# Kernel tuning notes

Measured on AMD Instinct MI355X. Metric: run time of the kernel, lower is better.

The kernel has to match this reference:

```python
import jax, jax.numpy as jnp
import numpy as np

E = 1024
H = 16
D = E // H
T = 1024
S = 1024
B = 8
MASK_FILL = 1e-30  # note: module fills masked scores with 1e-30, NOT -inf


def setup_inputs() -> dict:
    key = jax.random.key(0)
    ks = jax.random.split(key, 8)
    inp = {
        "query1": jax.random.normal(ks[0], (T, B, E), jnp.float32),
        "query2": jax.random.normal(ks[1], (T, B, E), jnp.float32),
        "key": jax.random.normal(ks[2], (S, B, E), jnp.float32),
        "value": jax.random.normal(ks[3], (S, B, E), jnp.float32),
        # causal mask: True = masked
        "attn_mask": jnp.triu(jnp.ones((T, S), jnp.bool_), k=1),
        # xavier-uniform-ish weights (torch stores Linear weight as [out, in])
        "q_w": jax.random.uniform(ks[4], (E, E), jnp.float32, -1, 1) * np.sqrt(6.0 / (2 * E)),
        "k_w": jax.random.uniform(ks[5], (E, E), jnp.float32, -1, 1) * np.sqrt(6.0 / (2 * E)),
        "v_w": jax.random.uniform(ks[6], (E, E), jnp.float32, -1, 1) * np.sqrt(6.0 / (2 * E)),
        "out_w": jax.random.uniform(ks[7], (E, E), jnp.float32, -1, 1) * np.sqrt(6.0 / (2 * E)),
    }
    return inp


def _split_heads(x):
    # [L, B, E] -> [B, H, L, D]
    L = x.shape[0]
    return x.reshape(L, B, H, D).transpose(1, 2, 0, 3)


def reference(query1, query2, key, value, attn_mask, q_w, k_w, v_w, out_w):
    scaling = float(D) ** -0.5
    q1 = _split_heads(query1 @ q_w.T) * scaling  # [B,H,T,D]
    q2 = _split_heads(query2 @ q_w.T) * scaling
    k = _split_heads(key @ k_w.T)                # [B,H,S,D]
    v = _split_heads(value @ v_w.T)

    # ---- stream s (second query stream attends first) ----
    scores_s = jnp.einsum("bhtd,bhsd->bhts", q2, k)
    scores_s = jnp.where(attn_mask[None, None], MASK_FILL, scores_s)
    probs_s = jax.nn.softmax(scores_s, axis=-1)
    o_s = jnp.einsum("bhts,bhsd->bhtd", probs_s, v)  # [B,H,T,D]

    # k/v update between passes (requires T == S)
    k2 = k + o_s
    v2 = v + o_s

    # ---- stream d ----
    scores_d = jnp.einsum("bhtd,bhsd->bhts", q1, k2)
    scores_d = jnp.where(attn_mask[None, None], MASK_FILL, scores_d)
    probs_d = jax.nn.softmax(scores_d, axis=-1)
    o_d = jnp.einsum("bhts,bhsd->bhtd", probs_d, v2)

    def _merge_and_proj(o):
        # [B,H,T,D] -> [T,B,E] -> out proj (no bias)
        return o.transpose(2, 0, 1, 3).reshape(T, B, E) @ out_w.T

    attn_output_s = _merge_and_proj(o_s)
    attn_output_d = _merge_and_proj(o_d)
    attn_s = probs_s.mean(axis=1)  # [B,T,S]
    attn_d = probs_d.mean(axis=1)
    return attn_output_d, attn_d, attn_output_s, attn_s
```

## Files before the change

kernel.cpp:

```cpp
#include <hip/hip_runtime.h>
#include <cstddef>

#define T_DIM 1024
#define S_DIM 1024
#define B_DIM 8
#define E_DIM 1024
#define H_DIM 16
#define D_DIM 64
#define NBHTD (B_DIM*H_DIM*T_DIM*D_DIM)

typedef __attribute__((ext_vector_type(8))) short short8;
typedef __attribute__((ext_vector_type(4))) short short4v;
typedef __attribute__((ext_vector_type(4))) float floatx4;

__device__ inline unsigned short f2bf(float x){
    union { float f; unsigned u; } v; v.f = x;
    unsigned r = (v.u + 0x7FFFu + ((v.u >> 16) & 1u)) >> 16;
    return (unsigned short)r;
}
__device__ inline float bf2f(unsigned short h){
    union { float f; unsigned u; } v; v.u = ((unsigned)h) << 16; return v.f;
}

typedef __attribute__((address_space(1))) const unsigned int* gptr_t;
typedef __attribute__((address_space(3))) unsigned int* lptr_t;
__device__ inline void gl_lds16(const void* g, void* l){
    __builtin_amdgcn_global_load_lds((gptr_t)g, (lptr_t)l, 16, 0, 0);
}

__device__ inline int poff(int row, int s){
    return (row << 10) + ((((s >> 3) ^ (row & 7)) << 3)) + (s & 7);
}

__global__ __launch_bounds__(256)
void split_pair(const float* __restrict__ src, unsigned short* __restrict__ hi,
                unsigned short* __restrict__ lo, float scale)
{
    size_t i = ((size_t)blockIdx.x*256 + threadIdx.x)*8;
    float4 a = *(const float4*)(src+i);
    float4 b = *(const float4*)(src+i+4);
    float v[8] = {a.x,a.y,a.z,a.w,b.x,b.y,b.z,b.w};
    short8 h8, l8;
    #pragma unroll
    for (int j = 0; j < 8; ++j) {
        float x = v[j]*scale;
        unsigned short hh = f2bf(x);
        h8[j] = (short)hh;
        l8[j] = (short)f2bf(x - bf2f(hh));
    }
    *(short8*)(hi+i) = h8;
    *(short8*)(lo+i) = l8;
}

template <int AMODE, int CMODE>
__global__ __launch_bounds__(256, 2)
void gemm_bf3(const unsigned short* __restrict__ Ahi, const unsigned short* __restrict__ Alo,
              const unsigned short* __restrict__ Bhi, const unsigned short* __restrict__ Blo,
              float* __restrict__ Cf,
              unsigned short* __restrict__ Chi, unsigned short* __restrict__ Clo)
{
    __shared__ __align__(16) unsigned short lds[4][128*32];

    const int tid  = threadIdx.x;
    const int n0   = blockIdx.x * 128;
    const int m0   = blockIdx.y * 128;
    const int wave = tid >> 6, lane = tid & 63;
    const int lrow = lane & 15, quad = lane >> 4;
    const int mw = (wave & 1)*64, nw = (wave >> 1)*64;

    floatx4 acc[4][4];
    #pragma unroll
    for (int i = 0; i < 4; ++i)
        #pragma unroll
        for (int j = 0; j < 4; ++j) acc[i][j] = (floatx4){0.f,0.f,0.f,0.f};

    for (int kk = 0; kk < 1024; kk += 32) {
        __syncthreads();
        #pragma unroll
        for (int rnd = 0; rnd < 2; ++rnd) {
            int c = rnd*256 + tid;
            int row = c >> 2, col8 = (c & 3)*8;
            size_t aoff;
            if (AMODE == 0) {
                aoff = (size_t)(m0+row)*1024 + kk + col8;
            } else {
                int r = m0 + row; int t = r >> 3, bb = r & 7;
                int h = kk >> 6, d0 = (kk & 63) + col8;
                aoff = (((size_t)(bb*H_DIM + h)*T_DIM) + t)*D_DIM + d0;
            }
            size_t boff = (size_t)(n0+row)*1024 + kk + col8;
            gl_lds16(Ahi + aoff, &lds[0][c*8]);
            gl_lds16(Alo + aoff, &lds[1][c*8]);
            gl_lds16(Bhi + boff, &lds[2][c*8]);
            gl_lds16(Blo + boff, &lds[3][c*8]);
        }
        __syncthreads();

        short8 ah[4], al[4], bh[4], bl[4];
        #pragma unroll
        for (int mt = 0; mt < 4; ++mt) {
            int r = mw + mt*16 + lrow;
            ah[mt] = *(const short8*)&lds[0][r*32 + quad*8];
            al[mt] = *(const short8*)&lds[1][r*32 + quad*8];
        }
        #pragma unroll
        for (int nt = 0; nt < 4; ++nt) {
            int r = nw + nt*16 + lrow;
            bh[nt] = *(const short8*)&lds[2][r*32 + quad*8];
            bl[nt] = *(const short8*)&lds[3][r*32 + quad*8];
        }
        #pragma unroll
        for (int mt = 0; mt < 4; ++mt)
            #pragma unroll
            for (int nt = 0; nt < 4; ++nt) {
                acc[mt][nt] = __builtin_amdgcn_mfma_f32_16x16x32_bf16(ah[mt], bh[nt], acc[mt][nt], 0,0,0);
                acc[mt][nt] = __builtin_amdgcn_mfma_f32_16x16x32_bf16(ah[mt], bl[nt], acc[mt][nt], 0,0,0);
                acc[mt][nt] = __builtin_amdgcn_mfma_f32_16x16x32_bf16(al[mt], bh[nt], acc[mt][nt], 0,0,0);
            }
    }

    #pragma unroll
    for (int mt = 0; mt < 4; ++mt) {
        #pragma unroll
        for (int nt = 0; nt < 4; ++nt) {
            int n = n0 + nw + nt*16 + lrow;
            #pragma unroll
            for (int r = 0; r < 4; ++r) {
                int m = m0 + mw + mt*16 + quad*4 + r;
                float v = acc[mt][nt][r];
                if (CMODE == 2) {
                    Cf[(size_t)m*1024 + n] = v;
                } else {
                    int t = m >> 3, bb = m & 7;
                    int h = n >> 6, d = n & 63;
                    size_t idx = (((size_t)(bb*H_DIM + h)*T_DIM) + t)*D_DIM + d;
                    if (CMODE == 0) {
                        Cf[idx] = v;
                    } else {
                        unsigned short hh = f2bf(v);
                        Chi[idx] = hh;
                        Clo[idx] = f2bf(v - bf2f(hh));
                    }
                }
            }
        }
    }
}

__global__ __launch_bounds__(256)
void split_vt(const float* __restrict__ Vh, unsigned short* __restrict__ Vthi,
              unsigned short* __restrict__ Vtlo)
{
    __shared__ float tile[64][68];
    const int bh = blockIdx.y, s0 = blockIdx.x*64;
    const int tid = threadIdx.x;
    const size_t base = (size_t)bh*S_DIM*D_DIM;

    {
        int r = tid >> 2, c0 = (tid & 3) * 16;
        const float* p = Vh + base + (size_t)(s0 + r)*D_DIM + c0;
        float4 a = *(const float4*)p;
        float4 b = *(const float4*)(p+4);
        float4 c = *(const float4*)(p+8);
        float4 d = *(const float4*)(p+12);
        *(float4*)&tile[r][c0]    = a;
        *(float4*)&tile[r][c0+4]  = b;
        *(float4*)&tile[r][c0+8]  = c;
        *(float4*)&tile[r][c0+12] = d;
    }
    __syncthreads();
    {
        int d = tid >> 2, cs = (tid & 3) * 16;
        short8 hi[2], lo[2];
        #pragma unroll
        for (int half = 0; half < 2; ++half)
            #pragma unroll
            for (int u = 0; u < 8; ++u) {
                float x = tile[cs + half*8 + u][d];
                unsigned short hh = f2bf(x);
                hi[half][u] = (short)hh;
                lo[half][u] = (short)f2bf(x - bf2f(hh));
            }
        size_t obase = base + (size_t)d*S_DIM + s0 + cs;
        *(short8*)(Vthi + obase)     = hi[0];
        *(short8*)(Vthi + obase + 8) = hi[1];
        *(short8*)(Vtlo + obase)     = lo[0];
        *(short8*)(Vtlo + obase + 8) = lo[1];
    }
}

__global__ __launch_bounds__(512, 4)
void attn_mfma(const float* __restrict__ Qh,
               const unsigned short* __restrict__ Khi, const unsigned short* __restrict__ Klo,
               const unsigned short* __restrict__ Vthi, const unsigned short* __restrict__ Vtlo,
               unsigned short* __restrict__ Ohi, unsigned short* __restrict__ Olo,
               float* __restrict__ mean0, float* __restrict__ mean1)
{
    const int bid = blockIdx.x;
    const int b   = bid & 7;
    const int t0  = ((bid >> 3) & 63) * 16;
    const int hh  = bid >> 9;
    const int tid  = threadIdx.x;
    const int lane = tid & 63;
    const int wave = tid >> 6;
    const int lrow = lane & 15;
    const int quad = lane >> 4;
    const int t_g  = t0 + lrow;

    __shared__ __align__(16) unsigned short plds[16*1024];
    __shared__ float  stats[8][16];
    __shared__ float  pbuf[4][16][16];

    float accm[32];
    #pragma unroll
    for (int i = 0; i < 32; ++i) accm[i] = 0.f;

    #pragma unroll 1
    for (int h = hh*8; h < hh*8 + 8; ++h) {
        const int bh = b*H_DIM + h;
        const size_t kbase = (size_t)bh * S_DIM * D_DIM;

        short8 qh0, ql0, qh1, ql1;
        {
            const float* qp = Qh + kbase + (size_t)(t0 + lrow)*D_DIM + quad*8;
            float4 a  = *(const float4*)qp;
            float4 b4 = *(const float4*)(qp+4);
            float4 c4 = *(const float4*)(qp+32);
            float4 d4 = *(const float4*)(qp+36);
            float va[8]  = {a.x,a.y,a.z,a.w,b4.x,b4.y,b4.z,b4.w};
            float vb8[8] = {c4.x,c4.y,c4.z,c4.w,d4.x,d4.y,d4.z,d4.w};
            #pragma unroll
            for (int j = 0; j < 8; ++j) {
                unsigned short h0 = f2bf(va[j]);
                qh0[j] = (short)h0; ql0[j] = (short)f2bf(va[j] - bf2f(h0));
                unsigned short h1 = f2bf(vb8[j]);
                qh1[j] = (short)h1; ql1[j] = (short)f2bf(vb8[j] - bf2f(h1));
            }
        }

        float sv[32];
        float sum_loc = 0.f;
        {
            const unsigned short* kph = Khi + kbase + (size_t)(wave*128 + lrow)*D_DIM + quad*8;
            const unsigned short* kpl = Klo + kbase + (size_t)(wave*128 + lrow)*D_DIM + quad*8;
            short8 kh0 = *(const short8*)(kph);
            short8 kh1 = *(const short8*)(kph + 32);
            short8 kl0 = *(const short8*)(kpl);
            short8 kl1 = *(const short8*)(kpl + 32);
            #pragma unroll
            for (int jt = 0; jt < 8; ++jt) {
                short8 nh0, nh1, nl0, nl1;
                if (jt < 7) {
                    const unsigned short* nph = kph + (jt+1)*16*D_DIM;
                    const unsigned short* npl = kpl + (jt+1)*16*D_DIM;
                    nh0 = *(const short8*)(nph);
                    nh1 = *(const short8*)(nph + 32);
                    nl0 = *(const short8*)(npl);
                    nl1 = *(const short8*)(npl + 32);
                }
                floatx4 acc = {0.f,0.f,0.f,0.f};
                acc = __builtin_amdgcn_mfma_f32_16x16x32_bf16(kh0, qh0, acc, 0,0,0);
                acc = __builtin_amdgcn_mfma_f32_16x16x32_bf16(kh1, qh1, acc, 0,0,0);
                acc = __builtin_amdgcn_mfma_f32_16x16x32_bf16(kl0, qh0, acc, 0,0,0);
                acc = __builtin_amdgcn_mfma_f32_16x16x32_bf16(kl1, qh1, acc, 0,0,0);
                acc = __builtin_amdgcn_mfma_f32_16x16x32_bf16(kh0, ql0, acc, 0,0,0);
                acc = __builtin_amdgcn_mfma_f32_16x16x32_bf16(kh1, ql1, acc, 0,0,0);
                const int sb = wave*128 + jt*16 + quad*4;
                #pragma unroll
                for (int r = 0; r < 4; ++r) {
                    float sval = (sb + r > t_g) ? 1e-30f : acc[r];
                    float p = __expf(sval);
                    sv[jt*4+r] = p;
                    sum_loc += p;
                }
                kh0 = nh0; kh1 = nh1; kl0 = nl0; kl1 = nl1;
            }
        }

        sum_loc += __shfl_xor(sum_loc, 16);
        sum_loc += __shfl_xor(sum_loc, 32);
        if (quad == 0) stats[wave][lrow] = sum_loc;
        __syncthreads();

        float sum_g = ((stats[0][lrow] + stats[1][lrow]) + (stats[2][lrow] + stats[3][lrow]))
                    + ((stats[4][lrow] + stats[5][lrow]) + (stats[6][lrow] + stats[7][lrow]));
        const float inv = 1.0f / sum_g;

        #pragma unroll
        for (int jt = 0; jt < 8; ++jt) {
            float p0 = sv[jt*4+0]*inv, p1 = sv[jt*4+1]*inv;
            float p2 = sv[jt*4+2]*inv, p3 = sv[jt*4+3]*inv;
            accm[jt*4+0] += p0; accm[jt*4+1] += p1;
            accm[jt*4+2] += p2; accm[jt*4+3] += p3;
            short4v pk;
            pk[0] = (short)f2bf(p0); pk[1] = (short)f2bf(p1);
            pk[2] = (short)f2bf(p2); pk[3] = (short)f2bf(p3);
            const int sidx = wave*128 + jt*16 + quad*4;
            *(short4v*)&plds[poff(lrow, sidx)] = pk;
        }
        __syncthreads();

        {
            const int d0    = (wave & 3)*16;
            const int shalf = (wave >> 2)*512;
            const unsigned short* vh = Vthi + kbase + (size_t)(d0 + lrow)*S_DIM;
            const unsigned short* vl = Vtlo + kbase + (size_t)(d0 + lrow)*S_DIM;
            floatx4 oa = {0.f,0.f,0.f,0.f}, ob = {0.f,0.f,0.f,0.f};
            #pragma unroll 4
            for (int sk = 0; sk < 512; sk += 32) {
                const int sa = shalf + sk + quad*8;
                short8 af  = *(const short8*)&plds[poff(lrow, sa)];
                short8 bh8 = *(const short8*)(vh + sa);
                short8 bl8 = *(const short8*)(vl + sa);
                oa = __builtin_amdgcn_mfma_f32_16x16x32_bf16(af, bh8, oa, 0,0,0);
                ob = __builtin_amdgcn_mfma_f32_16x16x32_bf16(af, bl8, ob, 0,0,0);
            }
            if (wave >= 4) {
                #pragma unroll
                for (int r = 0; r < 4; ++r)
                    pbuf[wave-4][quad*4+r][lrow] = oa[r] + ob[r];
            }
            __syncthreads();
            if (wave < 4) {
                #pragma unroll
                for (int r = 0; r < 4; ++r) {
                    int q = quad*4 + r;
                    float v = oa[r] + ob[r] + pbuf[wave][q][lrow];
                    size_t idx = kbase + (size_t)(t0+q)*D_DIM + d0 + lrow;
                    unsigned short hv = f2bf(v);
                    Ohi[idx] = hv;
                    Olo[idx] = f2bf(v - bf2f(hv));
                }
            }
        }
    }

    {
        float* mp = (hh ? mean1 : mean0)
                  + ((size_t)b*T_DIM + t_g)*S_DIM + wave*128 + quad*4;
        #pragma unroll
        for (int jt = 0; jt < 8; ++jt) {
            float4 p4;
            p4.x = accm[jt*4+0];
            p4.y = accm[jt*4+1];
            p4.z = accm[jt*4+2];
            p4.w = accm[jt*4+3];
            *(float4*)(mp + jt*16) = p4;
        }
    }
}

__global__ __launch_bounds__(256)
void merge_mean(float* __restrict__ dst, const float* __restrict__ part)
{
    size_t i = ((size_t)blockIdx.x*256 + threadIdx.x)*4;
    float4 a = *(const float4*)(dst+i);
    float4 b = *(const float4*)(part+i);
    a.x = (a.x+b.x)*0.0625f; a.y = (a.y+b.y)*0.0625f;
    a.z = (a.z+b.z)*0.0625f; a.w = (a.w+b.w)*0.0625f;
    *(float4*)(dst+i) = a;
}

__global__ __launch_bounds__(256)
void add_k(unsigned short* __restrict__ Khi, unsigned short* __restrict__ Klo,
           const unsigned short* __restrict__ Ohi, const unsigned short* __restrict__ Olo)
{
    size_t i = ((size_t)blockIdx.x*256 + threadIdx.x)*8;
    short8 hi = *(short8*)(Khi+i), lo = *(short8*)(Klo+i);
    short8 oh = *(const short8*)(Ohi+i), ol = *(const short8*)(Olo+i);
    short8 nh, nl;
    #pragma unroll
    for (int j = 0; j < 8; ++j) {
        float o = bf2f((unsigned short)oh[j]) + bf2f((unsigned short)ol[j]);
        float k = bf2f((unsigned short)hi[j]) + bf2f((unsigned short)lo[j]) + o;
        unsigned short hv = f2bf(k);
        nh[j] = (short)hv;
        nl[j] = (short)f2bf(k - bf2f(hv));
    }
    *(short8*)(Khi+i) = nh;
    *(short8*)(Klo+i) = nl;
}

__global__ __launch_bounds__(256)
void add_v(float* __restrict__ V,
           const unsigned short* __restrict__ Ohi, const unsigned short* __restrict__ Olo)
{
    size_t i = ((size_t)blockIdx.x*256 + threadIdx.x)*8;
    short8 oh = *(const short8*)(Ohi+i), ol = *(const short8*)(Olo+i);
    float4 v0 = *(const float4*)(V+i), v1 = *(const float4*)(V+i+4);
    float v[8] = {v0.x,v0.y,v0.z,v0.w,v1.x,v1.y,v1.z,v1.w};
    #pragma unroll
    for (int j = 0; j < 8; ++j)
        v[j] += bf2f((unsigned short)oh[j]) + bf2f((unsigned short)ol[j]);
    v0.x=v[0]; v0.y=v[1]; v0.z=v[2]; v0.w=v[3];
    v1.x=v[4]; v1.y=v[5]; v1.z=v[6]; v1.w=v[7];
    *(float4*)(V+i)   = v0;
    *(float4*)(V+i+4) = v1;
}

extern "C" void kernel_launch(void* const* d_in, const int* in_sizes, int n_in,
                              void* d_out, int out_size, void* d_ws, size_t ws_size,
                              hipStream_t stream)
{
    const float* q1  = (const float*)d_in[0];
    const float* q2  = (const float*)d_in[1];
    const float* key = (const float*)d_in[2];
    const float* val = (const float*)d_in[3];
    const float* qw  = (const float*)d_in[5];
    const float* kw  = (const float*)d_in[6];
    const float* vw  = (const float*)d_in[7];
    const float* ow  = (const float*)d_in[8];

    float* out   = (float*)d_out;
    float* outd  = out;
    float* attnd = out + 1*(size_t)NBHTD;
    float* outs  = out + 2*(size_t)NBHTD;
    float* attns = out + 3*(size_t)NBHTD;

    unsigned short* ws_u16 = (unsigned short*)d_ws;
    unsigned short* Khi  = ws_u16;
    unsigned short* Klo  = Khi  + (size_t)NBHTD;
    unsigned short* Vthi = Klo  + (size_t)NBHTD;
    unsigned short* Vtlo = Vthi + (size_t)NBHTD;
    unsigned short* R2a  = Vtlo + (size_t)NBHTD;
    unsigned short* R2b  = R2a  + 2*(size_t)NBHTD;

    const size_t EE = (size_t)E_DIM*E_DIM;
    unsigned short* qwhi = R2a;
    unsigned short* qwlo = qwhi + EE;
    unsigned short* kwhi = qwlo + EE;
    unsigned short* kwlo = kwhi + EE;
    unsigned short* vwhi = kwlo + EE;
    unsigned short* vwlo = vwhi + EE;
    float* Ms1f = (float*)R2a;
    unsigned short* Odhi = R2a;
    unsigned short* Odlo = Odhi + (size_t)NBHTD;
    unsigned short* Oshi = R2b;
    unsigned short* Oslo = Oshi + (size_t)NBHTD;
    unsigned short* owhi = ws_u16;
    unsigned short* owlo = owhi + EE;

    float* Q1h = outd;
    float* Q2h = outs;
    float* Vh  = attnd;
    unsigned short* Ahi = (unsigned short*)attns;
    unsigned short* Alo = Ahi + (size_t)NBHTD;

    const dim3 ggrid(8, 64);

    split_pair<<<512, 256, 0, stream>>>(qw, qwhi, qwlo, 1.f);
    split_pair<<<512, 256, 0, stream>>>(kw, kwhi, kwlo, 1.f);
    split_pair<<<512, 256, 0, stream>>>(vw, vwhi, vwlo, 1.f);

    split_pair<<<4096, 256, 0, stream>>>(key, Ahi, Alo, 1.f);
    gemm_bf3<0,1><<<ggrid, 256, 0, stream>>>(Ahi, Alo, kwhi, kwlo, nullptr, Khi, Klo);

    split_pair<<<4096, 256, 0, stream>>>(val, Ahi, Alo, 1.f);
    gemm_bf3<0,0><<<ggrid, 256, 0, stream>>>(Ahi, Alo, vwhi, vwlo, Vh, nullptr, nullptr);
    split_vt<<<dim3(16, 128), 256, 0, stream>>>(Vh, Vthi, Vtlo);

    split_pair<<<4096, 256, 0, stream>>>(q1, Ahi, Alo, 0.125f);
    gemm_bf3<0,0><<<ggrid, 256, 0, stream>>>(Ahi, Alo, qwhi, qwlo, Q1h, nullptr, nullptr);

    split_pair<<<4096, 256, 0, stream>>>(q2, Ahi, Alo, 0.125f);
    gemm_bf3<0,0><<<ggrid, 256, 0, stream>>>(Ahi, Alo, qwhi, qwlo, Q2h, nullptr, nullptr);

    attn_mfma<<<dim3(1024), 512, 0, stream>>>(Q2h, Khi, Klo, Vthi, Vtlo,
                                              Oshi, Oslo, attns, Ms1f);
    merge_mean<<<8192, 256, 0, stream>>>(attns, Ms1f);

    add_k<<<4096, 256, 0, stream>>>(Khi, Klo, Oshi, Oslo);
    add_v<<<4096, 256, 0, stream>>>(Vh, Oshi, Oslo);
    split_vt<<<dim3(16, 128), 256, 0, stream>>>(Vh, Vthi, Vtlo);

    attn_mfma<<<dim3(1024), 512, 0, stream>>>(Q1h, Khi, Klo, Vthi, Vtlo,
                                              Odhi, Odlo, attnd, outs);
    merge_mean<<<8192, 256, 0, stream>>>(attnd, outs);

    split_pair<<<512, 256, 0, stream>>>(ow, owhi, owlo, 1.f);
    gemm_bf3<1,2><<<ggrid, 256, 0, stream>>>(Oshi, Oslo, owhi, owlo, outs, nullptr, nullptr);
    gemm_bf3<1,2><<<ggrid, 256, 0, stream>>>(Odhi, Odlo, owhi, owlo, outd, nullptr, nullptr);
}
```

Before: 1.738 ms.

## Store unnormalized P as hi/lo bf16 in LDS and defer normalization

Unnormalized exp scores are split into hi/lo bf16 and written to two LDS buffers inside the QK loop. This drops the 32-float register array and one barrier. Normalization moves after the PV product, and a third MFMA (P_lo x V_hi) is added to improve accuracy. The cost is double the LDS footprint and traffic plus extra MFMA work, which may lower occupancy.

Result: no change. 1.763 ms (+1.4%).

```diff
diff --git a/kernel.cpp b/kernel.cpp
--- a/kernel.cpp
+++ b/kernel.cpp
@@ -207,7 +207,8 @@
     const int quad = lane >> 4;
     const int t_g  = t0 + lrow;
 
-    __shared__ __align__(16) unsigned short plds[16*1024];
+    __shared__ __align__(16) unsigned short phi[16*1024];
+    __shared__ __align__(16) unsigned short plo[16*1024];
     __shared__ float  stats[8][16];
     __shared__ float  pbuf[4][16][16];
 
@@ -238,7 +239,6 @@
             }
         }
 
-        float sv[32];
         float sum_loc = 0.f;
         {
             const unsigned short* kph = Khi + kbase + (size_t)(wave*128 + lrow)*D_DIM + quad*8;
@@ -266,13 +266,19 @@
                 acc = __builtin_amdgcn_mfma_f32_16x16x32_bf16(kh0, ql0, acc, 0,0,0);
                 acc = __builtin_amdgcn_mfma_f32_16x16x32_bf16(kh1, ql1, acc, 0,0,0);
                 const int sb = wave*128 + jt*16 + quad*4;
+                short4v pkh, pkl;
                 #pragma unroll
                 for (int r = 0; r < 4; ++r) {
                     float sval = (sb + r > t_g) ? 1e-30f : acc[r];
                     float p = __expf(sval);
-                    sv[jt*4+r] = p;
                     sum_loc += p;
+                    unsigned short hv = f2bf(p);
+                    pkh[r] = (short)hv;
+                    pkl[r] = (short)f2bf(p - bf2f(hv));
                 }
+                const int o = poff(lrow, sb);
+                *(short4v*)&phi[o] = pkh;
+                *(short4v*)&plo[o] = pkl;
                 kh0 = nh0; kh1 = nh1; kl0 = nl0; kl1 = nl1;
             }
         }
@@ -288,44 +294,46 @@
 
         #pragma unroll
         for (int jt = 0; jt < 8; ++jt) {
-            float p0 = sv[jt*4+0]*inv, p1 = sv[jt*4+1]*inv;
-            float p2 = sv[jt*4+2]*inv, p3 = sv[jt*4+3]*inv;
-            accm[jt*4+0] += p0; accm[jt*4+1] += p1;
-            accm[jt*4+2] += p2; accm[jt*4+3] += p3;
-            short4v pk;
-            pk[0] = (short)f2bf(p0); pk[1] = (short)f2bf(p1);
-            pk[2] = (short)f2bf(p2); pk[3] = (short)f2bf(p3);
-            const int sidx = wave*128 + jt*16 + quad*4;
-            *(short4v*)&plds[poff(lrow, sidx)] = pk;
-        }
-        __syncthreads();
+            const int sb = wave*128 + jt*16 + quad*4;
+            const int o = poff(lrow, sb);
+            short4v h4 = *(const short4v*)&phi[o];
+            short4v l4 = *(const short4v*)&plo[o];
+            #pragma unroll
+            for (int r = 0; r < 4; ++r)
+                accm[jt*4+r] += (bf2f((unsigned short)h4[r]) + bf2f((unsigned short)l4[r])) * inv;
+        }
 
         {
             const int d0    = (wave & 3)*16;
             const int shalf = (wave >> 2)*512;
             const unsigned short* vh = Vthi + kbase + (size_t)(d0 + lrow)*S_DIM;
             const unsigned short* vl = Vtlo + kbase + (size_t)(d0 + lrow)*S_DIM;
-            floatx4 oa = {0.f,0.f,0.f,0.f}, ob = {0.f,0.f,0.f,0.f};
+            floatx4 o1 = {0.f,0.f,0.f,0.f}, o2 = {0.f,0.f,0.f,0.f}, o3 = {0.f,0.f,0.f,0.f};
             #pragma unroll 4
             for (int sk = 0; sk < 512; sk += 32) {
                 const int sa = shalf + sk + quad*8;
-                short8 af  = *(const short8*)&plds[poff(lrow, sa)];
-                short8 bh8 = *(const short8*)(vh + sa);
-                short8 bl8 = *(const short8*)(vl + sa);
-                oa = __builtin_amdgcn_mfma_f32_16x16x32_bf16(af, bh8, oa, 0,0,0);
-                ob = __builtin_amdgcn_mfma_f32_16x16x32_bf16(af, bl8, ob, 0,0,0);
+                const int o = poff(lrow, sa);
+                short8 ph8 = *(const short8*)&phi[o];
+                short8 pl8 = *(const short8*)&plo[o];
+                short8 vh8 = *(const short8*)(vh + sa);
+                short8 vl8 = *(const short8*)(vl + sa);
+                o1 = __builtin_amdgcn_mfma_f32_16x16x32_bf16(ph8, vh8, o1, 0,0,0);
+                o2 = __builtin_amdgcn_mfma_f32_16x16x32_bf16(ph8, vl8, o2, 0,0,0);
+                o3 = __builtin_amdgcn_mfma_f32_16x16x32_bf16(pl8, vh8, o3, 0,0,0);
             }
             if (wave >= 4) {
                 #pragma unroll
-                for (int r = 0; r < 4; ++r)
-                    pbuf[wave-4][quad*4+r][lrow] = oa[r] + ob[r];
+                for (int r = 0; r < 4; ++r) {
+                    float vr = (o1[r] + o2[r] + o3[r]) * __shfl(inv, quad*4 + r);
+                    pbuf[wave-4][quad*4+r][lrow] = vr;
+                }
             }
             __syncthreads();
             if (wave < 4) {
                 #pragma unroll
                 for (int r = 0; r < 4; ++r) {
                     int q = quad*4 + r;
-                    float v = oa[r] + ob[r] + pbuf[wave][q][lrow];
+                    float v = (o1[r] + o2[r] + o3[r]) * __shfl(inv, q) + pbuf[wave][q][lrow];
                     size_t idx = kbase + (size_t)(t0+q)*D_DIM + d0 + lrow;
                     unsigned short hv = f2bf(v);
                     Ohi[idx] = hv;
```

## Process all heads per block and defer softmax normalization, drop merge_mean pass

Applied to the files above, without the earlier changes.

The attention kernel now uses 4-wave blocks that loop over all 16 heads for a 16-row tile, so the head-mean of probabilities builds up in registers and the separate merge_mean kernel with its partial buffer goes away. Unnormalized exp values are written straight to LDS as bf16 during the score loop, and the 1/sum scaling is applied to the PV output afterwards instead of before. K loads are double-buffered with explicit A/B register sets. The trade-off is half as many blocks with longer serial work, more accumulator registers (64 floats), and a head-mean now computed from bf16-rounded probabilities.

Result: slower. 2.028 ms (+16.7%).

```diff
diff --git a/kernel.cpp b/kernel.cpp
--- a/kernel.cpp
+++ b/kernel.cpp
@@ -189,36 +189,37 @@
     }
 }
 
-__global__ __launch_bounds__(512, 4)
+__global__ __launch_bounds__(256, 4)
 void attn_mfma(const float* __restrict__ Qh,
                const unsigned short* __restrict__ Khi, const unsigned short* __restrict__ Klo,
                const unsigned short* __restrict__ Vthi, const unsigned short* __restrict__ Vtlo,
                unsigned short* __restrict__ Ohi, unsigned short* __restrict__ Olo,
-               float* __restrict__ mean0, float* __restrict__ mean1)
+               float* __restrict__ attn_mean)
 {
     const int bid = blockIdx.x;
     const int b   = bid & 7;
-    const int t0  = ((bid >> 3) & 63) * 16;
-    const int hh  = bid >> 9;
+    const int t0  = (bid >> 3) * 16;
     const int tid  = threadIdx.x;
     const int lane = tid & 63;
     const int wave = tid >> 6;
     const int lrow = lane & 15;
     const int quad = lane >> 4;
     const int t_g  = t0 + lrow;
-
-    __shared__ __align__(16) unsigned short plds[16*1024];
-    __shared__ float  stats[8][16];
-    __shared__ float  pbuf[4][16][16];
-
-    float accm[32];
-    #pragma unroll
-    for (int i = 0; i < 32; ++i) accm[i] = 0.f;
+    const int s0   = wave * 256;
+
+    __shared__ __align__(16) unsigned short phi[16*1024];
+    __shared__ float stats[4][16];
+
+    float accm[64];
+    #pragma unroll
+    for (int i = 0; i < 64; ++i) accm[i] = 0.f;
 
     #pragma unroll 1
-    for (int h = hh*8; h < hh*8 + 8; ++h) {
+    for (int h = 0; h < H_DIM; ++h) {
         const int bh = b*H_DIM + h;
         const size_t kbase = (size_t)bh * S_DIM * D_DIM;
+
+        __syncthreads();
 
         short8 qh0, ql0, qh1, ql1;
         {
@@ -238,43 +239,52 @@
             }
         }
 
-        float sv[32];
         float sum_loc = 0.f;
         {
-            const unsigned short* kph = Khi + kbase + (size_t)(wave*128 + lrow)*D_DIM + quad*8;
-            const unsigned short* kpl = Klo + kbase + (size_t)(wave*128 + lrow)*D_DIM + quad*8;
-            short8 kh0 = *(const short8*)(kph);
-            short8 kh1 = *(const short8*)(kph + 32);
-            short8 kl0 = *(const short8*)(kpl);
-            short8 kl1 = *(const short8*)(kpl + 32);
-            #pragma unroll
-            for (int jt = 0; jt < 8; ++jt) {
-                short8 nh0, nh1, nl0, nl1;
-                if (jt < 7) {
-                    const unsigned short* nph = kph + (jt+1)*16*D_DIM;
-                    const unsigned short* npl = kpl + (jt+1)*16*D_DIM;
-                    nh0 = *(const short8*)(nph);
-                    nh1 = *(const short8*)(nph + 32);
-                    nl0 = *(const short8*)(npl);
-                    nl1 = *(const short8*)(npl + 32);
-                }
-                floatx4 acc = {0.f,0.f,0.f,0.f};
-                acc = __builtin_amdgcn_mfma_f32_16x16x32_bf16(kh0, qh0, acc, 0,0,0);
-                acc = __builtin_amdgcn_mfma_f32_16x16x32_bf16(kh1, qh1, acc, 0,0,0);
-                acc = __builtin_amdgcn_mfma_f32_16x16x32_bf16(kl0, qh0, acc, 0,0,0);
-                acc = __builtin_amdgcn_mfma_f32_16x16x32_bf16(kl1, qh1, acc, 0,0,0);
-                acc = __builtin_amdgcn_mfma_f32_16x16x32_bf16(kh0, ql0, acc, 0,0,0);
-                acc = __builtin_amdgcn_mfma_f32_16x16x32_bf16(kh1, ql1, acc, 0,0,0);
-                const int sb = wave*128 + jt*16 + quad*4;
-                #pragma unroll
-                for (int r = 0; r < 4; ++r) {
-                    float sval = (sb + r > t_g) ? 1e-30f : acc[r];
-                    float p = __expf(sval);
-                    sv[jt*4+r] = p;
-                    sum_loc += p;
-                }
-                kh0 = nh0; kh1 = nh1; kl0 = nl0; kl1 = nl1;
-            }
+            const unsigned short* kph = Khi + kbase + (size_t)(s0 + lrow)*D_DIM + quad*8;
+            const unsigned short* kpl = Klo + kbase + (size_t)(s0 + lrow)*D_DIM + quad*8;
+
+            #define LOADK(JT, C0, C1, C2, C3) do {                          \
+                const unsigned short* ph_ = kph + (JT)*16*D_DIM;            \
+                const unsigned short* pl_ = kpl + (JT)*16*D_DIM;            \
+                C0 = *(const short8*)(ph_);                                 \
+                C1 = *(const short8*)(ph_ + 32);                            \
+                C2 = *(const short8*)(pl_);                                 \
+                C3 = *(const short8*)(pl_ + 32);                            \
+            } while (0)
+
+            #define SCORE(JT, C0, C1, C2, C3) do {                          \
+                floatx4 acc_ = {0.f,0.f,0.f,0.f};                           \
+                acc_ = __builtin_amdgcn_mfma_f32_16x16x32_bf16(C0, qh0, acc_, 0,0,0); \
+                acc_ = __builtin_amdgcn_mfma_f32_16x16x32_bf16(C1, qh1, acc_, 0,0,0); \
+                acc_ = __builtin_amdgcn_mfma_f32_16x16x32_bf16(C2, qh0, acc_, 0,0,0); \
+                acc_ = __builtin_amdgcn_mfma_f32_16x16x32_bf16(C3, qh1, acc_, 0,0,0); \
+                acc_ = __builtin_amdgcn_mfma_f32_16x16x32_bf16(C0, ql0, acc_, 0,0,0); \
+                acc_ = __builtin_amdgcn_mfma_f32_16x16x32_bf16(C1, ql1, acc_, 0,0,0); \
+                const int sb_ = s0 + (JT)*16 + quad*4;                      \
+                short4v pk_;                                                \
+                _Pragma("unroll")                                           \
+                for (int r_ = 0; r_ < 4; ++r_) {                            \
+                    float sval_ = (sb_ + r_ > t_g) ? 1e-30f : acc_[r_];     \
+                    float p_ = __expf(sval_);                               \
+                    sum_loc += p_;                                          \
+                    pk_[r_] = (short)f2bf(p_);                              \
+                }                                                           \
+                *(short4v*)&phi[poff(lrow, sb_)] = pk_;                     \
+            } while (0)
+
+            short8 a0, a1, a2, a3, b0, b1, b2, b3;
+            LOADK(0, a0, a1, a2, a3);
+            LOADK(1, b0, b1, b2, b3);
+            #pragma unroll
+            for (int jt = 0; jt < 16; jt += 2) {
+                SCORE(jt, a0, a1, a2, a3);
+                if (jt + 2 < 16) LOADK(jt + 2, a0, a1, a2, a3);
+                SCORE(jt + 1, b0, b1, b2, b3);
+                if (jt + 3 < 16) LOADK(jt + 3, b0, b1, b2, b3);
+            }
+            #undef LOADK
+            #undef SCORE
         }
 
         sum_loc += __shfl_xor(sum_loc, 16);
@@ -282,83 +292,57 @@
         if (quad == 0) stats[wave][lrow] = sum_loc;
         __syncthreads();
 
-        float sum_g = ((stats[0][lrow] + stats[1][lrow]) + (stats[2][lrow] + stats[3][lrow]))
-                    + ((stats[4][lrow] + stats[5][lrow]) + (stats[6][lrow] + stats[7][lrow]));
+        const float sum_g = (stats[0][lrow] + stats[1][lrow])
+                          + (stats[2][lrow] + stats[3][lrow]);
         const float inv = 1.0f / sum_g;
 
         #pragma unroll
-        for (int jt = 0; jt < 8; ++jt) {
-            float p0 = sv[jt*4+0]*inv, p1 = sv[jt*4+1]*inv;
-            float p2 = sv[jt*4+2]*inv, p3 = sv[jt*4+3]*inv;
-            accm[jt*4+0] += p0; accm[jt*4+1] += p1;
-            accm[jt*4+2] += p2; accm[jt*4+3] += p3;
-            short4v pk;
-            pk[0] = (short)f2bf(p0); pk[1] = (short)f2bf(p1);
-            pk[2] = (short)f2bf(p2); pk[3] = (short)f2bf(p3);
-            const int sidx = wave*128 + jt*16 + quad*4;
-            *(short4v*)&plds[poff(lrow, sidx)] = pk;
-        }
-        __syncthreads();
+        for (int jt = 0; jt < 16; ++jt) {
+            const int sb = s0 + jt*16 + quad*4;
+            short4v h4 = *(const short4v*)&phi[poff(lrow, sb)];
+            #pragma unroll
+            for (int r = 0; r < 4; ++r)
+                accm[jt*4+r] += bf2f((unsigned short)h4[r]) * inv;
+        }
 
         {
-            const int d0    = (wave & 3)*16;
-            const int shalf = (wave >> 2)*512;
+            const int d0 = wave*16;
             const unsigned short* vh = Vthi + kbase + (size_t)(d0 + lrow)*S_DIM;
             const unsigned short* vl = Vtlo + kbase + (size_t)(d0 + lrow)*S_DIM;
-            floatx4 oa = {0.f,0.f,0.f,0.f}, ob = {0.f,0.f,0.f,0.f};
+            floatx4 o1 = {0.f,0.f,0.f,0.f}, o2 = {0.f,0.f,0.f,0.f};
             #pragma unroll 4
-            for (int sk = 0; sk < 512; sk += 32) {
-                const int sa = shalf + sk + quad*8;
-                short8 af  = *(const short8*)&plds[poff(lrow, sa)];
-                short8 bh8 = *(const short8*)(vh + sa);
-                short8 bl8 = *(const short8*)(vl + sa);
-                oa = __builtin_amdgcn_mfma_f32_16x16x32_bf16(af, bh8, oa, 0,0,0);
-                ob = __builtin_amdgcn_mfma_f32_16x16x32_bf16(af, bl8, ob, 0,0,0);
-            }
-            if (wave >= 4) {
-                #pragma unroll
-                for (int r = 0; r < 4; ++r)
-                    pbuf[wave-4][quad*4+r][lrow] = oa[r] + ob[r];
-            }
-            __syncthreads();
-            if (wave < 4) {
-                #pragma unroll
-                for (int r = 0; r < 4; ++r) {
-                    int q = quad*4 + r;
-                    float v = oa[r] + ob[r] + pbuf[wave][q][lrow];
-                    size_t idx = kbase + (size_t)(t0+q)*D_DIM + d0 + lrow;
-                    unsigned short hv = f2bf(v);
-                    Ohi[idx] = hv;
-                    Olo[idx] = f2bf(v - bf2f(hv));
-                }
+            for (int sk = 0; sk < S_DIM; sk += 32) {
+                const int sa = sk + quad*8;
+                short8 pf  = *(const short8*)&phi[poff(lrow, sa)];
+                short8 vh8 = *(const short8*)(vh + sa);
+                short8 vl8 = *(const short8*)(vl + sa);
+                o1 = __builtin_amdgcn_mfma_f32_16x16x32_bf16(pf, vh8, o1, 0,0,0);
+                o2 = __builtin_amdgcn_mfma_f32_16x16x32_bf16(pf, vl8, o2, 0,0,0);
+            }
+            #pragma unroll
+            for (int r = 0; r < 4; ++r) {
+                int q = quad*4 + r;
+                float v = (o1[r] + o2[r]) * __shfl(inv, q);
+                size_t idx = kbase + (size_t)(t0+q)*D_DIM + d0 + lrow;
+                unsigned short hv = f2bf(v);
+                Ohi[idx] = hv;
+                Olo[idx] = f2bf(v - bf2f(hv));
             }
         }
     }
 
     {
-        float* mp = (hh ? mean1 : mean0)
-                  + ((size_t)b*T_DIM + t_g)*S_DIM + wave*128 + quad*4;
-        #pragma unroll
-        for (int jt = 0; jt < 8; ++jt) {
+        float* am = attn_mean + ((size_t)b*T_DIM + t_g)*S_DIM + s0 + quad*4;
+        #pragma unroll
+        for (int jt = 0; jt < 16; ++jt) {
             float4 p4;
-            p4.x = accm[jt*4+0];
-            p4.y = accm[jt*4+1];
-            p4.z = accm[jt*4+2];
-            p4.w = accm[jt*4+3];
-            *(float4*)(mp + jt*16) = p4;
-        }
-    }
-}
-
-__global__ __launch_bounds__(256)
-void merge_mean(float* __restrict__ dst, const float* __restrict__ part)
-{
-    size_t i = ((size_t)blockIdx.x*256 + threadIdx.x)*4;
-    float4 a = *(const float4*)(dst+i);
-    float4 b = *(const float4*)(part+i);
-    a.x = (a.x+b.x)*0.0625f; a.y = (a.y+b.y)*0.0625f;
-    a.z = (a.z+b.z)*0.0625f; a.w = (a.w+b.w)*0.0625f;
-    *(float4*)(dst+i) = a;
+            p4.x = accm[jt*4+0]*(1.0f/H_DIM);
+            p4.y = accm[jt*4+1]*(1.0f/H_DIM);
+            p4.z = accm[jt*4+2]*(1.0f/H_DIM);
+            p4.w = accm[jt*4+3]*(1.0f/H_DIM);
+            *(float4*)(am + jt*16) = p4;
+        }
+    }
 }
 
 __global__ __launch_bounds__(256)
@@ -432,7 +416,6 @@
     unsigned short* kwlo = kwhi + EE;
     unsigned short* vwhi = kwlo + EE;
     unsigned short* vwlo = vwhi + EE;
-    float* Ms1f = (float*)R2a;
     unsigned short* Odhi = R2a;
     unsigned short* Odlo = Odhi + (size_t)NBHTD;
     unsigned short* Oshi = R2b;
@@ -465,17 +448,15 @@
     split_pair<<<4096, 256, 0, stream>>>(q2, Ahi, Alo, 0.125f);
     gemm_bf3<0,0><<<ggrid, 256, 0, stream>>>(Ahi, Alo, qwhi, qwlo, Q2h, nullptr, nullptr);
 
-    attn_mfma<<<dim3(1024), 512, 0, stream>>>(Q2h, Khi, Klo, Vthi, Vtlo,
-                                              Oshi, Oslo, attns, Ms1f);
-    merge_mean<<<8192, 256, 0, stream>>>(attns, Ms1f);
+    attn_mfma<<<dim3(512), 256, 0, stream>>>(Q2h, Khi, Klo, Vthi, Vtlo,
+                                             Oshi, Oslo, attns);
 
     add_k<<<4096, 256, 0, stream>>>(Khi, Klo, Oshi, Oslo);
     add_v<<<4096, 256, 0, stream>>>(Vh, Oshi, Oslo);
     split_vt<<<dim3(16, 128), 256, 0, stream>>>(Vh, Vthi, Vtlo);
 
-    attn_mfma<<<dim3(1024), 512, 0, stream>>>(Q1h, Khi, Klo, Vthi, Vtlo,
-                                              Odhi, Odlo, attnd, outs);
-    merge_mean<<<8192, 256, 0, stream>>>(attnd, outs);
+    attn_mfma<<<dim3(512), 256, 0, stream>>>(Q1h, Khi, Klo, Vthi, Vtlo,
+                                             Odhi, Odlo, attnd);
 
     split_pair<<<512, 256, 0, stream>>>(ow, owhi, owlo, 1.f);
     gemm_bf3<1,2><<<ggrid, 256, 0, stream>>>(Oshi, Oslo, owhi, owlo, outs, nullptr, nullptr);
```
